# Kernel tuning notes

Measured on AMD Instinct MI355X. Metric: run time of the kernel, lower is better.

The kernel has to match this reference:

```python
import jax, jax.numpy as jnp
import numpy as np

L = 48          # dialogue length (nodes)
D = 256         # global_feature_dim
H = 256         # rgcn.dim
G = 256         # gcn.dim
A = 128         # attention dim
R = 2 * L * L   # number of relation types


def setup_inputs() -> dict:
    key = jax.random.key(0)
    ks = jax.random.split(key, 12)
    rn = lambda k, shape, fan_in: (jax.random.normal(k, shape, jnp.float32)
                                   / np.float32(np.sqrt(fan_in)))
    return {
        "global_features": jax.random.normal(ks[0], (L, D), jnp.float32),
        "speaker": jax.random.randint(ks[1], (L,), 0, 2),
        # Bahdanau attention params: score = v . tanh(q Wq + k Wk)
        "Wq": rn(ks[2], (D, A), D),
        "Wk": rn(ks[3], (D, A), D),
        "v": rn(ks[4], (A,), A),
        # RGCN params: per-relation weights + root weight + bias
        "W_rel": rn(ks[5], (R, D, H), D),
        "W_root": rn(ks[6], (D, H), D),
        "b_rgcn": jnp.zeros((H,), jnp.float32),
        # GraphConv params: neighbor weight, root weight, bias
        "W_nbr": rn(ks[7], (H, G), H),
        "W_self": rn(ks[8], (H, G), H),
        "b_gcn": jnp.zeros((G,), jnp.float32),
    }


def reference(global_features, speaker, Wq, Wk, v, W_rel, W_root, b_rgcn,
              W_nbr, W_self, b_gcn):
    x = global_features                       # [L, D]
    n = x.shape[0]

    # ---- Bahdanau attention over all utterances (query i vs key t) ----
    q = x @ Wq                                # [L, A]
    k = x @ Wk                                # [L, A]
    scores = jnp.tanh(q[:, None, :] + k[None, :, :]) @ v   # [L, L]
    attn = jax.nn.softmax(scores, axis=-1)    # [L, L]
    edge_weight = attn.reshape(-1)            # [L*L], row-major matches edge order

    # ---- fully-connected edge list: (i, j) for i in range(L) for j in range(L)
    src = jnp.repeat(jnp.arange(n), n)        # [E] source i
    dst = jnp.tile(jnp.arange(n), n)          # [E] target j
    direction = jnp.where(src < dst, 0, 1)    # i<j -> 0 else 1
    # edge_type id of key f'{sp_i}{sp_j}{dir}' in enumeration order
    etype = 2 * (speaker[src] * n + speaker[dst]) + direction  # [E]

    # ---- RGCNConv: per-relation transform, edge-weighted scatter-add ----
    # msg_e = w_e * (x[src_e] @ W_rel[etype_e])
    msg = jnp.einsum('ed,edh->eh', x[src], W_rel[etype]) * edge_weight[:, None]
    agg = jax.ops.segment_sum(msg, dst, num_segments=n)       # [L, H]
    h = agg + x @ W_root + b_rgcn                              # [L, H]

    # ---- GraphConv: out_i = W_self h_i + W_nbr sum_{j->i} h_j + b ----
    nbr = jax.ops.segment_sum(h[src], dst, num_segments=n)    # [L, H]
    out = h @ W_self + nbr @ W_nbr + b_gcn                     # [L, G]
    return out
```

## Files before the change

kernel.cpp:

```cpp
#include <hip/hip_runtime.h>
#include <hip/hip_bf16.h>

#define NL 48
#define ND 256
#define NH 256
#define NG 256
#define NA 128

__global__ void qk_kernel(const float* __restrict__ x,
                          const float* __restrict__ Wq,
                          const float* __restrict__ Wk,
                          float* __restrict__ q, float* __restrict__ k) {
    int i = blockIdx.x;
    int a = threadIdx.x;
    __shared__ float xs[ND];
    xs[a]        = x[i * ND + a];
    xs[a + 128]  = x[i * ND + a + 128];
    __syncthreads();
    float accq = 0.f, acck = 0.f;
    #pragma unroll 8
    for (int d = 0; d < ND; ++d) {
        float xv = xs[d];
        accq += xv * Wq[d * NA + a];
        acck += xv * Wk[d * NA + a];
    }
    q[i * NA + a] = accq;
    k[i * NA + a] = acck;
}

__global__ void attn_kernel(const float* __restrict__ q,
                            const float* __restrict__ k,
                            const float* __restrict__ v,
                            float* __restrict__ attn) {
    int i = blockIdx.x;
    int j = threadIdx.x;
    __shared__ float qs[NA];
    __shared__ float vs[NA];
    qs[j]      = q[i * NA + j];
    qs[j + 64] = q[i * NA + j + 64];
    vs[j]      = v[j];
    vs[j + 64] = v[j + 64];
    __syncthreads();

    float s = -INFINITY;
    if (j < NL) {
        float sc = 0.f;
        #pragma unroll 8
        for (int a = 0; a < NA; ++a)
            sc += vs[a] * tanhf(qs[a] + k[j * NA + a]);
        s = sc;
    }
    float m = s;
    for (int off = 32; off; off >>= 1) m = fmaxf(m, __shfl_xor(m, off));
    float e = (j < NL) ? __expf(s - m) : 0.f;
    float tot = e;
    for (int off = 32; off; off >>= 1) tot += __shfl_xor(tot, off);
    if (j < NL) attn[i * NL + j] = e / tot;
}

__global__ void y_kernel(const float* __restrict__ x,
                         const int* __restrict__ speaker,
                         const float* __restrict__ W_rel,
                         float* __restrict__ y) {
    int blk = blockIdx.x;
    int i = blk >> 2;
    int c = blk & 3;
    int hh = threadIdx.x;
    __shared__ float xs[ND];
    xs[hh] = x[i * ND + hh];
    __syncthreads();
    int si  = speaker[i];
    int rid = 2 * (si * NL + (c >> 1)) + (c & 1);
    const float* W = W_rel + (size_t)rid * ND * NH;
    float acc = 0.f;
    #pragma unroll 8
    for (int d = 0; d < ND; ++d)
        acc += xs[d] * W[d * NH + hh];
    y[(i * 4 + c) * NH + hh] = acc;
}

__global__ void h_kernel(const float* __restrict__ x,
                         const int* __restrict__ speaker,
                         const float* __restrict__ W_root,
                         const float* __restrict__ b_rgcn,
                         const float* __restrict__ attn,
                         const float* __restrict__ y,
                         float* __restrict__ h) {
    int j = blockIdx.x;
    int hh = threadIdx.x;
    __shared__ float xs[ND];
    __shared__ float wcol[NL];
    xs[hh] = x[j * ND + hh];
    if (hh < NL) wcol[hh] = attn[hh * NL + j];
    __syncthreads();

    int sj = speaker[j];
    float acc = b_rgcn[hh];
    for (int i = 0; i < NL; ++i) {
        int c = sj * 2 + ((i < j) ? 0 : 1);
        acc += wcol[i] * y[(i * 4 + c) * NH + hh];
    }
    #pragma unroll 8
    for (int d = 0; d < ND; ++d)
        acc += xs[d] * W_root[d * NH + hh];
    h[j * NH + hh] = acc;
}

__global__ void sumh_kernel(const float* __restrict__ h, float* __restrict__ sumh) {
    int hh = threadIdx.x;
    float acc = 0.f;
    #pragma unroll
    for (int j = 0; j < NL; ++j) acc += h[j * NH + hh];
    sumh[hh] = acc;
}

__global__ void out_kernel(const float* __restrict__ h,
                           const float* __restrict__ sumh,
                           const float* __restrict__ W_self,
                           const float* __restrict__ W_nbr,
                           const float* __restrict__ b_gcn,
                           float* __restrict__ out) {
    int j = blockIdx.x;
    int g = threadIdx.x;
    __shared__ float hs[NH];
    __shared__ float ss[NH];
    hs[g] = h[j * NH + g];
    ss[g] = sumh[g];
    __syncthreads();
    float acc = b_gcn[g];
    #pragma unroll 8
    for (int d = 0; d < NH; ++d) {
        acc += hs[d] * W_self[d * NG + g];
        acc += ss[d] * W_nbr[d * NG + g];
    }
    out[j * NG + g] = acc;
}

extern "C" void kernel_launch(void* const* d_in, const int* in_sizes, int n_in,
                              void* d_out, int out_size, void* d_ws, size_t ws_size,
                              hipStream_t stream) {
    const float* x      = (const float*)d_in[0];
    const int*   speaker= (const int*)d_in[1];
    const float* Wq     = (const float*)d_in[2];
    const float* Wk     = (const float*)d_in[3];
    const float* v      = (const float*)d_in[4];
    const float* W_rel  = (const float*)d_in[5];
    const float* W_root = (const float*)d_in[6];
    const float* b_rgcn = (const float*)d_in[7];
    const float* W_nbr  = (const float*)d_in[8];
    const float* W_self = (const float*)d_in[9];
    const float* b_gcn  = (const float*)d_in[10];
    float* out = (float*)d_out;

    float* ws   = (float*)d_ws;
    float* q    = ws;
    float* k    = q    + NL * NA;
    float* attn = k    + NL * NA;
    float* y    = attn + NL * NL;
    float* h    = y    + NL * 4 * NH;
    float* sumh = h    + NL * NH;

    qk_kernel  <<<NL,     128, 0, stream>>>(x, Wq, Wk, q, k);
    attn_kernel<<<NL,      64, 0, stream>>>(q, k, v, attn);
    y_kernel   <<<NL * 4, 256, 0, stream>>>(x, speaker, W_rel, y);
    h_kernel   <<<NL,     256, 0, stream>>>(x, speaker, W_root, b_rgcn, attn, y, h);
    sumh_kernel<<<1,      256, 0, stream>>>(h, sumh);
    out_kernel <<<NL,     256, 0, stream>>>(h, sumh, W_self, W_nbr, b_gcn, out);
}
```

Baseline: 1.366 ms.

## Fuse all stages into one cooperative kernel with grid syncs

Replaces six separate kernel launches with a single cooperative kernel of 192 blocks. Grid-wide syncs separate the phases: q/k plus relation transforms, attention softmax, RGCN aggregation, and GraphConv output. The q/k projection now runs alongside the W_rel transform in the first phase, and the column sum of h is recomputed per block instead of in a separate one-block kernel. The goal is to remove launch overhead and inter-kernel gaps, at the cost of grid-sync overhead and redundant column sums.

After: 1.456 ms. 6.6% more time.

```diff
diff --git a/kernel.cpp b/kernel.cpp
--- a/kernel.cpp
+++ b/kernel.cpp
@@ -1,5 +1,7 @@
 #include <hip/hip_runtime.h>
-#include <hip/hip_bf16.h>
+#include <hip/hip_cooperative_groups.h>
+
+namespace cg = cooperative_groups;
 
 #define NL 48
 #define ND 256
@@ -7,133 +9,117 @@
 #define NG 256
 #define NA 128
 
-__global__ void qk_kernel(const float* __restrict__ x,
-                          const float* __restrict__ Wq,
-                          const float* __restrict__ Wk,
-                          float* __restrict__ q, float* __restrict__ k) {
-    int i = blockIdx.x;
-    int a = threadIdx.x;
-    __shared__ float xs[ND];
-    xs[a]        = x[i * ND + a];
-    xs[a + 128]  = x[i * ND + a + 128];
-    __syncthreads();
-    float accq = 0.f, acck = 0.f;
-    #pragma unroll 8
-    for (int d = 0; d < ND; ++d) {
-        float xv = xs[d];
-        accq += xv * Wq[d * NA + a];
-        acck += xv * Wk[d * NA + a];
+__global__ void __launch_bounds__(256, 1) fused_dialoguegcn(
+    const float* __restrict__ x,      const int* __restrict__ speaker,
+    const float* __restrict__ Wq,     const float* __restrict__ Wk,
+    const float* __restrict__ v,      const float* __restrict__ W_rel,
+    const float* __restrict__ W_root, const float* __restrict__ b_rgcn,
+    const float* __restrict__ W_nbr,  const float* __restrict__ W_self,
+    const float* __restrict__ b_gcn,
+    float* __restrict__ q, float* __restrict__ k, float* __restrict__ attn,
+    float* __restrict__ y, float* __restrict__ h, float* __restrict__ out)
+{
+    cg::grid_group grid = cg::this_grid();
+    const int b = blockIdx.x;
+    const int t = threadIdx.x;
+    __shared__ float smem[2 * ND];
+
+    {
+        const int i = b >> 2;
+        const int c = b & 3;
+        float* xs = smem;
+        float* xq = smem + ND;
+        xs[t] = x[i * ND + t];
+        if (b < NL) xq[t] = x[b * ND + t];
+        __syncthreads();
+
+        const int rid = 2 * (speaker[i] * NL + (c >> 1)) + (c & 1);
+        const float* W = W_rel + (size_t)rid * ND * NH;
+        float acc = 0.f;
+        #pragma unroll 8
+        for (int d = 0; d < ND; ++d)
+            acc += xs[d] * W[d * NH + t];
+        y[(i * 4 + c) * NH + t] = acc;
+
+        if (b < NL) {
+            const float* Wqk = (t < NA) ? Wq : Wk;
+            const int a = t & (NA - 1);
+            float accq = 0.f;
+            #pragma unroll 8
+            for (int d = 0; d < ND; ++d)
+                accq += xq[d] * Wqk[d * NA + a];
+            float* qk = (t < NA) ? q : k;
+            qk[b * NA + a] = accq;
+        }
     }
-    q[i * NA + a] = accq;
-    k[i * NA + a] = acck;
-}
+    grid.sync();
 
-__global__ void attn_kernel(const float* __restrict__ q,
-                            const float* __restrict__ k,
-                            const float* __restrict__ v,
-                            float* __restrict__ attn) {
-    int i = blockIdx.x;
-    int j = threadIdx.x;
-    __shared__ float qs[NA];
-    __shared__ float vs[NA];
-    qs[j]      = q[i * NA + j];
-    qs[j + 64] = q[i * NA + j + 64];
-    vs[j]      = v[j];
-    vs[j + 64] = v[j + 64];
-    __syncthreads();
+    if (b < NL && t < 64) {
+        const int i = b, j = t;
+        float* qs = smem;
+        float* vs = smem + NA;
+        qs[j]      = q[i * NA + j];
+        qs[j + 64] = q[i * NA + j + 64];
+        vs[j]      = v[j];
+        vs[j + 64] = v[j + 64];
 
-    float s = -INFINITY;
-    if (j < NL) {
-        float sc = 0.f;
+        float s = -INFINITY;
+        if (j < NL) {
+            float sc = 0.f;
+            #pragma unroll 8
+            for (int a = 0; a < NA; ++a)
+                sc += vs[a] * tanhf(qs[a] + k[j * NA + a]);
+            s = sc;
+        }
+        float m = s;
+        for (int off = 32; off; off >>= 1) m = fmaxf(m, __shfl_xor(m, off));
+        float e = (j < NL) ? __expf(s - m) : 0.f;
+        float tot = e;
+        for (int off = 32; off; off >>= 1) tot += __shfl_xor(tot, off);
+        if (j < NL) attn[i * NL + j] = e / tot;
+    }
+    grid.sync();
+
+    if (b < NL) {
+        const int j = b;
+        float* xs   = smem;
+        float* wcol = smem + ND;
+        xs[t] = x[j * ND + t];
+        if (t < NL) wcol[t] = attn[t * NL + j];
+        __syncthreads();
+
+        const int sj = speaker[j];
+        float acc = b_rgcn[t];
+        for (int i = 0; i < NL; ++i) {
+            const int c = sj * 2 + ((i < j) ? 0 : 1);
+            acc += wcol[i] * y[(i * 4 + c) * NH + t];
+        }
         #pragma unroll 8
-        for (int a = 0; a < NA; ++a)
-            sc += vs[a] * tanhf(qs[a] + k[j * NA + a]);
-        s = sc;
+        for (int d = 0; d < ND; ++d)
+            acc += xs[d] * W_root[d * NH + t];
+        h[j * NH + t] = acc;
     }
-    float m = s;
-    for (int off = 32; off; off >>= 1) m = fmaxf(m, __shfl_xor(m, off));
-    float e = (j < NL) ? __expf(s - m) : 0.f;
-    float tot = e;
-    for (int off = 32; off; off >>= 1) tot += __shfl_xor(tot, off);
-    if (j < NL) attn[i * NL + j] = e / tot;
-}
+    grid.sync();
 
-__global__ void y_kernel(const float* __restrict__ x,
-                         const int* __restrict__ speaker,
-                         const float* __restrict__ W_rel,
-                         float* __restrict__ y) {
-    int blk = blockIdx.x;
-    int i = blk >> 2;
-    int c = blk & 3;
-    int hh = threadIdx.x;
-    __shared__ float xs[ND];
-    xs[hh] = x[i * ND + hh];
-    __syncthreads();
-    int si  = speaker[i];
-    int rid = 2 * (si * NL + (c >> 1)) + (c & 1);
-    const float* W = W_rel + (size_t)rid * ND * NH;
-    float acc = 0.f;
-    #pragma unroll 8
-    for (int d = 0; d < ND; ++d)
-        acc += xs[d] * W[d * NH + hh];
-    y[(i * 4 + c) * NH + hh] = acc;
-}
+    if (b < NL) {
+        const int j = b;
+        float* hs = smem;
+        float* ss = smem + NH;
+        hs[t] = h[j * NH + t];
+        float s = 0.f;
+        #pragma unroll
+        for (int jj = 0; jj < NL; ++jj) s += h[jj * NH + t];
+        ss[t] = s;
+        __syncthreads();
 
-__global__ void h_kernel(const float* __restrict__ x,
-                         const int* __restrict__ speaker,
-                         const float* __restrict__ W_root,
-                         const float* __restrict__ b_rgcn,
-                         const float* __restrict__ attn,
-                         const float* __restrict__ y,
-                         float* __restrict__ h) {
-    int j = blockIdx.x;
-    int hh = threadIdx.x;
-    __shared__ float xs[ND];
-    __shared__ float wcol[NL];
-    xs[hh] = x[j * ND + hh];
-    if (hh < NL) wcol[hh] = attn[hh * NL + j];
-    __syncthreads();
-
-    int sj = speaker[j];
-    float acc = b_rgcn[hh];
-    for (int i = 0; i < NL; ++i) {
-        int c = sj * 2 + ((i < j) ? 0 : 1);
-        acc += wcol[i] * y[(i * 4 + c) * NH + hh];
+        float acc = b_gcn[t];
+        #pragma unroll 8
+        for (int d = 0; d < NH; ++d) {
+            acc += hs[d] * W_self[d * NG + t];
+            acc += ss[d] * W_nbr[d * NG + t];
+        }
+        out[j * NG + t] = acc;
     }
-    #pragma unroll 8
-    for (int d = 0; d < ND; ++d)
-        acc += xs[d] * W_root[d * NH + hh];
-    h[j * NH + hh] = acc;
-}
-
-__global__ void sumh_kernel(const float* __restrict__ h, float* __restrict__ sumh) {
-    int hh = threadIdx.x;
-    float acc = 0.f;
-    #pragma unroll
-    for (int j = 0; j < NL; ++j) acc += h[j * NH + hh];
-    sumh[hh] = acc;
-}
-
-__global__ void out_kernel(const float* __restrict__ h,
-                           const float* __restrict__ sumh,
-                           const float* __restrict__ W_self,
-                           const float* __restrict__ W_nbr,
-                           const float* __restrict__ b_gcn,
-                           float* __restrict__ out) {
-    int j = blockIdx.x;
-    int g = threadIdx.x;
-    __shared__ float hs[NH];
-    __shared__ float ss[NH];
-    hs[g] = h[j * NH + g];
-    ss[g] = sumh[g];
-    __syncthreads();
-    float acc = b_gcn[g];
-    #pragma unroll 8
-    for (int d = 0; d < NH; ++d) {
-        acc += hs[d] * W_self[d * NG + g];
-        acc += ss[d] * W_nbr[d * NG + g];
-    }
-    out[j * NG + g] = acc;
 }
 
 extern "C" void kernel_launch(void* const* d_in, const int* in_sizes, int n_in,
@@ -158,12 +144,13 @@
     float* attn = k    + NL * NA;
     float* y    = attn + NL * NL;
     float* h    = y    + NL * 4 * NH;
-    float* sumh = h    + NL * NH;
 
-    qk_kernel  <<<NL,     128, 0, stream>>>(x, Wq, Wk, q, k);
-    attn_kernel<<<NL,      64, 0, stream>>>(q, k, v, attn);
-    y_kernel   <<<NL * 4, 256, 0, stream>>>(x, speaker, W_rel, y);
-    h_kernel   <<<NL,     256, 0, stream>>>(x, speaker, W_root, b_rgcn, attn, y, h);
-    sumh_kernel<<<1,      256, 0, stream>>>(h, sumh);
-    out_kernel <<<NL,     256, 0, stream>>>(h, sumh, W_self, W_nbr, b_gcn, out);
+    void* args[] = {
+        (void*)&x, (void*)&speaker, (void*)&Wq, (void*)&Wk, (void*)&v,
+        (void*)&W_rel, (void*)&W_root, (void*)&b_rgcn, (void*)&W_nbr,
+        (void*)&W_self, (void*)&b_gcn,
+        (void*)&q, (void*)&k, (void*)&attn, (void*)&y, (void*)&h, (void*)&out
+    };
+    hipLaunchCooperativeKernel((void*)fused_dialoguegcn,
+                               dim3(192), dim3(256), args, 0, stream);
 }
```
